# Kernel tuning notes

Hardware: AMD Instinct MI355X
Metric: run time of the kernel (lower is better)

## Reference

```python
import jax, jax.numpy as jnp
import numpy as np

N_NODES, FEAT, EMB, BATCH, NUM_SAMPLE = 100000, 256, 256, 10000, 32


def setup_inputs() -> dict:
    key = jax.random.key(0)
    ks = jax.random.split(key, 8)
    sc = 1.0 / np.sqrt(FEAT).astype(np.float32)
    return {
        "nodes": jax.random.randint(ks[0], (BATCH,), 0, N_NODES),
        "neigh_idx": jax.random.randint(ks[1], (BATCH, NUM_SAMPLE), 0, N_NODES),
        "id2feat": jax.random.normal(ks[2], (N_NODES, FEAT), jnp.float32),
        "Wq": jax.random.normal(ks[3], (FEAT, EMB), jnp.float32) * sc,
        "bq": jnp.zeros((EMB,), jnp.float32),
        "Wk": jax.random.normal(ks[4], (FEAT, EMB), jnp.float32) * sc,
        "bk": jnp.zeros((EMB,), jnp.float32),
        "Wv": jax.random.normal(ks[5], (FEAT, EMB), jnp.float32) * sc,
        "bv": jnp.zeros((EMB,), jnp.float32),
    }


def reference(nodes, neigh_idx, id2feat, Wq, bq, Wk, bk, Wv, bv):
    # Gather: self feats [B, F] and sampled neighbor feats [B, S, F]
    self_feats = id2feat[nodes]
    neigh_feats = id2feat[neigh_idx]
    S = neigh_idx.shape[1]
    # Keys/values over [neighbors, self] -> [B, S+1, F]
    cat = jnp.concatenate([neigh_feats, self_feats[:, None, :]], axis=1)
    Q = self_feats @ Wq + bq               # [B, E]
    K = cat @ Wk + bk                       # [B, S+1, E]
    V = cat @ Wv + bv                       # [B, S+1, E]
    scores = jnp.einsum('be,bse->bs', Q, K)  # [B, S+1]
    # Faithful to original mask loop: with full neighbor lists, columns >= num_sample
    # (the appended self key) are masked out.
    mask = jnp.arange(S + 1) >= S
    scores = jnp.where(mask[None, :], -jnp.inf, scores)
    attn = jax.nn.softmax(scores, axis=-1)   # [B, S+1]
    return jnp.einsum('bs,bse->be', attn, V)  # [B, E]
```

## Files before the change

kernel.cpp:

```cpp
#include <hip/hip_runtime.h>
#include <math.h>

#define F 256
#define E 256
#define S 32
#define CH 4
#define NB 16
#define TLP 260

typedef __attribute__((ext_vector_type(8))) short short8;
typedef __attribute__((ext_vector_type(4))) float f32x4;

__device__ __forceinline__ ushort f2bf(float x) {
    uint u = __float_as_uint(x);
    return (ushort)((u + 0x7fffu + ((u >> 16) & 1u)) >> 16);
}
__device__ __forceinline__ float bf2f(ushort h) {
    return __uint_as_float(((uint)h) << 16);
}
__device__ __forceinline__ uint4 pack8(const ushort* h) {
    uint4 r;
    r.x = (uint)h[0] | ((uint)h[1] << 16); r.y = (uint)h[2] | ((uint)h[3] << 16);
    r.z = (uint)h[4] | ((uint)h[5] << 16); r.w = (uint)h[6] | ((uint)h[7] << 16);
    return r;
}
__device__ __forceinline__ void split8(const float* x, short8& h, short8& l) {
    ushort hh[8], ll[8];
#pragma unroll
    for (int i = 0; i < 8; ++i) { hh[i] = f2bf(x[i]); ll[i] = f2bf(x[i] - bf2f(hh[i])); }
    uint4 ph = pack8(hh), pl = pack8(ll);
    h = *reinterpret_cast<short8*>(&ph);
    l = *reinterpret_cast<short8*>(&pl);
}
__device__ __forceinline__ short8 mk8(uint a, uint b, uint c, uint d) {
    uint4 p = make_uint4(a, b, c, d);
    return *reinterpret_cast<short8*>(&p);
}
__device__ __forceinline__ uint pkbf(float v) {
    const ushort h = f2bf(v);
    const ushort l = f2bf(v - bf2f(h));
    return (uint)h | ((uint)l << 16);
}

__global__ __launch_bounds__(512) void prep(const float* __restrict__ Wq,
                                            const float* __restrict__ bq,
                                            const float* __restrict__ Wk,
                                            const float* __restrict__ Wv,
                                            ushort* __restrict__ MTh,
                                            ushort* __restrict__ MTl,
                                            ushort* __restrict__ WvTh,
                                            ushort* __restrict__ WvTl,
                                            float* __restrict__ c) {
    const int blk = blockIdx.x, tid = threadIdx.x;
    const int lane = tid & 63, wave = tid >> 6;
    if (blk < 4) {
        const int wm = wave >> 2, wn = wave & 3;
        const int fr = lane & 15, fk = lane >> 4;
        const int j0 = blk * 64;
        f32x4 acc[2][4];
#pragma unroll
        for (int m = 0; m < 2; ++m)
#pragma unroll
            for (int n = 0; n < 4; ++n) acc[m][n] = (f32x4){0.f, 0.f, 0.f, 0.f};
        for (int k0 = 0; k0 < F; k0 += 32) {
            short8 ah[2], al[2];
#pragma unroll
            for (int m = 0; m < 2; ++m) {
                const float* p = &Wk[(size_t)(j0 + wm * 32 + m * 16 + fr) * F + k0 + fk * 8];
                float x[8];
                *reinterpret_cast<float4*>(&x[0]) = *reinterpret_cast<const float4*>(p);
                *reinterpret_cast<float4*>(&x[4]) = *reinterpret_cast<const float4*>(p + 4);
                split8(x, ah[m], al[m]);
            }
#pragma unroll
            for (int n = 0; n < 4; ++n) {
                const float* p = &Wq[(size_t)(wn * 64 + n * 16 + fr) * F + k0 + fk * 8];
                float x[8];
                *reinterpret_cast<float4*>(&x[0]) = *reinterpret_cast<const float4*>(p);
                *reinterpret_cast<float4*>(&x[4]) = *reinterpret_cast<const float4*>(p + 4);
                short8 bh, bl;
                split8(x, bh, bl);
#pragma unroll
                for (int m = 0; m < 2; ++m) {
                    acc[m][n] = __builtin_amdgcn_mfma_f32_16x16x32_bf16(ah[m], bh, acc[m][n], 0, 0, 0);
                    acc[m][n] = __builtin_amdgcn_mfma_f32_16x16x32_bf16(ah[m], bl, acc[m][n], 0, 0, 0);
                    acc[m][n] = __builtin_amdgcn_mfma_f32_16x16x32_bf16(al[m], bh, acc[m][n], 0, 0, 0);
                }
            }
        }
#pragma unroll
        for (int n = 0; n < 4; ++n) {
            const int i = wn * 64 + n * 16 + fr;
#pragma unroll
            for (int m = 0; m < 2; ++m)
#pragma unroll
                for (int r = 0; r < 4; ++r) {
                    const int j = j0 + wm * 32 + m * 16 + fk * 4 + r;
                    const float v = acc[m][n][r];
                    const ushort h = f2bf(v);
                    MTh[(size_t)j * F + i] = h;
                    MTl[(size_t)j * F + i] = f2bf(v - bf2f(h));
                }
        }
    } else if (blk < 20) {
        __shared__ float t[64][65];
        const int tb = blk - 4;
        const int jt = (tb & 3) * 64, kt = (tb >> 2) * 64;
        const int lk = tid >> 3, lj = (tid & 7) * 8;
        {
            const float* p = &Wv[(size_t)(kt + lk) * E + jt + lj];
            const float4 v0 = *reinterpret_cast<const float4*>(p);
            const float4 v1 = *reinterpret_cast<const float4*>(p + 4);
            t[lk][lj + 0] = v0.x; t[lk][lj + 1] = v0.y; t[lk][lj + 2] = v0.z; t[lk][lj + 3] = v0.w;
            t[lk][lj + 4] = v1.x; t[lk][lj + 5] = v1.y; t[lk][lj + 6] = v1.z; t[lk][lj + 7] = v1.w;
        }
        __syncthreads();
        const int oj = tid >> 3, ok = (tid & 7) * 8;
        ushort h[8], l[8];
#pragma unroll
        for (int u = 0; u < 8; ++u) {
            const float v = t[ok + u][oj];
            h[u] = f2bf(v); l[u] = f2bf(v - bf2f(h[u]));
        }
        *reinterpret_cast<uint4*>(&WvTh[(size_t)(jt + oj) * F + kt + ok]) = pack8(h);
        *reinterpret_cast<uint4*>(&WvTl[(size_t)(jt + oj) * F + kt + ok]) = pack8(l);
    } else {
        __shared__ float bqs[F];
        if (tid < F) bqs[tid] = bq[tid];
        __syncthreads();
        const float4 b4 = *reinterpret_cast<const float4*>(&bqs[lane * 4]);
#pragma unroll
        for (int i = 0; i < 8; ++i) {
            const int j = (blk - 20) * 64 + wave * 8 + i;
            const float4 k4 = *reinterpret_cast<const float4*>(&Wk[(size_t)j * F + lane * 4]);
            float p = k4.x * b4.x + k4.y * b4.y + k4.z * b4.z + k4.w * b4.w;
#pragma unroll
            for (int off = 32; off; off >>= 1) p += __shfl_xor(p, off);
            if (lane == 0) c[j] = p;
        }
    }
}

__device__ __forceinline__ void ld_chunk(float4* d, int idxv, int s0,
                                         const float* __restrict__ t, int lane) {
#pragma unroll
    for (int j = 0; j < CH; ++j) {
        const int nid = __builtin_amdgcn_readlane(idxv, s0 + j);
        d[j] = *reinterpret_cast<const float4*>(&t[(size_t)nid * F + lane * 4]);
    }
}
__device__ __forceinline__ void proc_chunk(const float4* v, const float4 qv,
                                           float& m, float& l, float4& acc) {
#pragma unroll
    for (int j = 0; j < CH; ++j) {
        float p = v[j].x * qv.x + v[j].y * qv.y + v[j].z * qv.z + v[j].w * qv.w;
#pragma unroll
        for (int off = 32; off; off >>= 1) p += __shfl_xor(p, off);
        if (p <= m) {
            const float w = __expf(p - m);
            l += w;
            acc.x += w * v[j].x; acc.y += w * v[j].y;
            acc.z += w * v[j].z; acc.w += w * v[j].w;
        } else {
            const float cc = __expf(m - p);
            l = l * cc + 1.f;
            acc.x = acc.x * cc + v[j].x; acc.y = acc.y * cc + v[j].y;
            acc.z = acc.z * cc + v[j].z; acc.w = acc.w * cc + v[j].w;
            m = p;
        }
    }
}

__global__ __launch_bounds__(256) void fused(const int* __restrict__ nodes,
                                             const int* __restrict__ neigh,
                                             const float* __restrict__ id2feat,
                                             const ushort* __restrict__ MTh,
                                             const ushort* __restrict__ MTl,
                                             const ushort* __restrict__ WvTh,
                                             const ushort* __restrict__ WvTl,
                                             const float* __restrict__ cb,
                                             const float* __restrict__ bv,
                                             float* __restrict__ out,
                                             int B) {
    __shared__ uint tile[NB][TLP];

    const int tid = threadIdx.x;
    const int lane = tid & 63, wave = tid >> 6;
    const int fr = lane & 15, fk = lane >> 4;
    const int row0 = blockIdx.x * NB;

    const int gr = row0 + fr;
    const int arow = nodes[gr < B ? gr : B - 1];

    f32x4 acc[4];
#pragma unroll
    for (int n = 0; n < 4; ++n) acc[n] = (f32x4){0.f, 0.f, 0.f, 0.f};

    for (int k0 = 0; k0 < F; k0 += 32) {
        const float* p = id2feat + (size_t)arow * F + k0 + fk * 8;
        float x[8];
        *reinterpret_cast<float4*>(&x[0]) = *reinterpret_cast<const float4*>(p);
        *reinterpret_cast<float4*>(&x[4]) = *reinterpret_cast<const float4*>(p + 4);
        short8 ah, al;
        split8(x, ah, al);
#pragma unroll
        for (int n = 0; n < 4; ++n) {
            const size_t boff = (size_t)(wave * 64 + n * 16 + fr) * F + k0 + fk * 8;
            const short8 bh = *reinterpret_cast<const short8*>(&MTh[boff]);
            const short8 bl = *reinterpret_cast<const short8*>(&MTl[boff]);
            acc[n] = __builtin_amdgcn_mfma_f32_16x16x32_bf16(ah, bh, acc[n], 0, 0, 0);
            acc[n] = __builtin_amdgcn_mfma_f32_16x16x32_bf16(ah, bl, acc[n], 0, 0, 0);
            acc[n] = __builtin_amdgcn_mfma_f32_16x16x32_bf16(al, bh, acc[n], 0, 0, 0);
        }
    }
#pragma unroll
    for (int n = 0; n < 4; ++n) {
        const int col = wave * 64 + n * 16 + fr;
        const float cc = cb[col];
#pragma unroll
        for (int r = 0; r < 4; ++r)
            tile[fk * 4 + r][col] = __float_as_uint(acc[n][r] + cc);
    }
    __syncthreads();

#pragma unroll 1
    for (int i = 0; i < 4; ++i) {
        const int tr = wave * 4 + i;
        const int node = row0 + tr;
        if (node < B) {
            const int idxv = neigh[node * S + (lane & (S - 1))];
            const uint4 q4 = *reinterpret_cast<const uint4*>(&tile[tr][lane * 4]);
            const float4 qv = make_float4(__uint_as_float(q4.x), __uint_as_float(q4.y),
                                          __uint_as_float(q4.z), __uint_as_float(q4.w));
            float m = -INFINITY, l = 0.f;
            float4 a = make_float4(0.f, 0.f, 0.f, 0.f);
            float4 va[CH], vb[CH];
            ld_chunk(va, idxv, 0, id2feat, lane);
            ld_chunk(vb, idxv, 4, id2feat, lane);
            proc_chunk(va, qv, m, l, a);
            ld_chunk(va, idxv, 8, id2feat, lane);
            proc_chunk(vb, qv, m, l, a);
            ld_chunk(vb, idxv, 12, id2feat, lane);
            proc_chunk(va, qv, m, l, a);
            ld_chunk(va, idxv, 16, id2feat, lane);
            proc_chunk(vb, qv, m, l, a);
            ld_chunk(vb, idxv, 20, id2feat, lane);
            proc_chunk(va, qv, m, l, a);
            ld_chunk(va, idxv, 24, id2feat, lane);
            proc_chunk(vb, qv, m, l, a);
            ld_chunk(vb, idxv, 28, id2feat, lane);
            proc_chunk(va, qv, m, l, a);
            proc_chunk(vb, qv, m, l, a);
            const float inv = 1.0f / l;
            const uint4 o = make_uint4(pkbf(a.x * inv), pkbf(a.y * inv),
                                       pkbf(a.z * inv), pkbf(a.w * inv));
            *reinterpret_cast<uint4*>(&tile[tr][lane * 4]) = o;
        }
    }
    __syncthreads();

#pragma unroll
    for (int n = 0; n < 4; ++n) acc[n] = (f32x4){0.f, 0.f, 0.f, 0.f};

    for (int k0 = 0; k0 < F; k0 += 32) {
        const uint4 u0 = *reinterpret_cast<const uint4*>(&tile[fr][k0 + fk * 8]);
        const uint4 u1 = *reinterpret_cast<const uint4*>(&tile[fr][k0 + fk * 8 + 4]);
        const short8 ah = mk8((u0.x & 0xffffu) | (u0.y << 16), (u0.z & 0xffffu) | (u0.w << 16),
                              (u1.x & 0xffffu) | (u1.y << 16), (u1.z & 0xffffu) | (u1.w << 16));
        const short8 al = mk8((u0.x >> 16) | (u0.y & 0xffff0000u), (u0.z >> 16) | (u0.w & 0xffff0000u),
                              (u1.x >> 16) | (u1.y & 0xffff0000u), (u1.z >> 16) | (u1.w & 0xffff0000u));
#pragma unroll
        for (int n = 0; n < 4; ++n) {
            const size_t boff = (size_t)(wave * 64 + n * 16 + fr) * F + k0 + fk * 8;
            const short8 bh = *reinterpret_cast<const short8*>(&WvTh[boff]);
            const short8 bl = *reinterpret_cast<const short8*>(&WvTl[boff]);
            acc[n] = __builtin_amdgcn_mfma_f32_16x16x32_bf16(ah, bh, acc[n], 0, 0, 0);
            acc[n] = __builtin_amdgcn_mfma_f32_16x16x32_bf16(ah, bl, acc[n], 0, 0, 0);
            acc[n] = __builtin_amdgcn_mfma_f32_16x16x32_bf16(al, bh, acc[n], 0, 0, 0);
        }
    }
#pragma unroll
    for (int n = 0; n < 4; ++n) {
        const int col = wave * 64 + n * 16 + fr;
        const float bb = bv[col];
#pragma unroll
        for (int r = 0; r < 4; ++r) {
            const int grow = row0 + fk * 4 + r;
            if (grow < B) out[(size_t)grow * E + col] = acc[n][r] + bb;
        }
    }
}

extern "C" void kernel_launch(void* const* d_in, const int* in_sizes, int n_in,
                              void* d_out, int out_size, void* d_ws, size_t ws_size,
                              hipStream_t stream) {
    const int*   nodes   = (const int*)d_in[0];
    const int*   neigh   = (const int*)d_in[1];
    const float* id2feat = (const float*)d_in[2];
    const float* Wq      = (const float*)d_in[3];
    const float* bq      = (const float*)d_in[4];
    const float* Wk      = (const float*)d_in[5];
    const float* Wv      = (const float*)d_in[7];
    const float* bv      = (const float*)d_in[8];
    float* out = (float*)d_out;
    const int B = in_sizes[0];

    ushort* MTh  = (ushort*)d_ws;
    ushort* MTl  = MTh + 65536;
    ushort* WvTh = MTl + 65536;
    ushort* WvTl = WvTh + 65536;
    float*  cbuf = (float*)(WvTl + 65536);

    prep<<<dim3(24), dim3(512), 0, stream>>>(Wq, bq, Wk, Wv, MTh, MTl, WvTh, WvTl, cbuf);
    fused<<<dim3((B + NB - 1) / NB), dim3(256), 0, stream>>>(nodes, neigh, id2feat,
                                                             MTh, MTl, WvTh, WvTl,
                                                             cbuf, bv, out, B);
}
```

Before: 124.7 us.

## Split fused kernel into tiled Q GEMM and per-node gather/attention kernel

Replaces the single fused kernel with two kernels. The first is a tiled GEMM that computes the transformed query for every batch node, staging A tiles in double-buffered LDS, and writes it to workspace. The second handles one node per wave for the online-softmax gather, then runs the Wv projection on 4-row tiles. That projection drops the Wv low-part MFMA term, which lowers precision. The aim is better occupancy and latency hiding for the gather phase, at the cost of a workspace round trip and MFMA tiles where only 4 of 16 rows carry data.

```diff
diff --git a/kernel.cpp b/kernel.cpp
--- a/kernel.cpp
+++ b/kernel.cpp
@@ -5,8 +5,6 @@
 #define E 256
 #define S 32
 #define CH 4
-#define NB 16
-#define TLP 260
 
 typedef __attribute__((ext_vector_type(8))) short short8;
 typedef __attribute__((ext_vector_type(4))) float f32x4;
@@ -23,6 +21,13 @@
     r.x = (uint)h[0] | ((uint)h[1] << 16); r.y = (uint)h[2] | ((uint)h[3] << 16);
     r.z = (uint)h[4] | ((uint)h[5] << 16); r.w = (uint)h[6] | ((uint)h[7] << 16);
     return r;
+}
+__device__ __forceinline__ void split4(const float* x, uint2& ph, uint2& pl) {
+    ushort h[4], l[4];
+#pragma unroll
+    for (int i = 0; i < 4; ++i) { h[i] = f2bf(x[i]); l[i] = f2bf(x[i] - bf2f(h[i])); }
+    ph.x = (uint)h[0] | ((uint)h[1] << 16); ph.y = (uint)h[2] | ((uint)h[3] << 16);
+    pl.x = (uint)l[0] | ((uint)l[1] << 16); pl.y = (uint)l[2] | ((uint)l[3] << 16);
 }
 __device__ __forceinline__ void split8(const float* x, short8& h, short8& l) {
     ushort hh[8], ll[8];
@@ -141,6 +146,83 @@
     }
 }
 
+__global__ __launch_bounds__(256) void qgemm(const float* __restrict__ X,
+                                             const int* __restrict__ nodes,
+                                             const ushort* __restrict__ BTh,
+                                             const ushort* __restrict__ BTl,
+                                             const float* __restrict__ cb,
+                                             float* __restrict__ outq,
+                                             int B) {
+    __shared__ ushort Ah[2][32][40], Al[2][32][40];
+    const int tid = threadIdx.x, lane = tid & 63, wave = tid >> 6;
+    const int fr = lane & 15, fk = lane >> 4;
+    const int row0 = blockIdx.x * 32;
+    const int col0 = blockIdx.y * 128 + wave * 32;
+
+    const int arL = tid >> 3, akL = (tid & 7) * 4;
+    const int gr = row0 + arL;
+    const int grc = gr < B ? gr : B - 1;
+    const float* aptr = X + (size_t)nodes[grc] * F + akL;
+
+    f32x4 acc[2][2];
+#pragma unroll
+    for (int m = 0; m < 2; ++m)
+#pragma unroll
+        for (int n = 0; n < 2; ++n) acc[m][n] = (f32x4){0.f, 0.f, 0.f, 0.f};
+
+    {
+        const float4 av = *reinterpret_cast<const float4*>(aptr);
+        uint2 h, l; split4(&av.x, h, l);
+        *reinterpret_cast<uint2*>(&Ah[0][arL][akL]) = h;
+        *reinterpret_cast<uint2*>(&Al[0][arL][akL]) = l;
+    }
+    __syncthreads();
+
+    for (int t = 0; t < 8; ++t) {
+        const int cur = t & 1;
+        float4 nv;
+        if (t < 7) nv = *reinterpret_cast<const float4*>(aptr + (t + 1) * 32);
+
+        short8 a_h[2], a_l[2];
+#pragma unroll
+        for (int m = 0; m < 2; ++m) {
+            a_h[m] = *reinterpret_cast<const short8*>(&Ah[cur][m * 16 + fr][fk * 8]);
+            a_l[m] = *reinterpret_cast<const short8*>(&Al[cur][m * 16 + fr][fk * 8]);
+        }
+#pragma unroll
+        for (int n = 0; n < 2; ++n) {
+            const size_t boff = (size_t)(col0 + n * 16 + fr) * F + t * 32 + fk * 8;
+            const short8 bh = *reinterpret_cast<const short8*>(&BTh[boff]);
+            const short8 bl = *reinterpret_cast<const short8*>(&BTl[boff]);
+#pragma unroll
+            for (int m = 0; m < 2; ++m) {
+                acc[m][n] = __builtin_amdgcn_mfma_f32_16x16x32_bf16(a_h[m], bh, acc[m][n], 0, 0, 0);
+                acc[m][n] = __builtin_amdgcn_mfma_f32_16x16x32_bf16(a_h[m], bl, acc[m][n], 0, 0, 0);
+                acc[m][n] = __builtin_amdgcn_mfma_f32_16x16x32_bf16(a_l[m], bh, acc[m][n], 0, 0, 0);
+            }
+        }
+        if (t < 7) {
+            uint2 h, l; split4(&nv.x, h, l);
+            *reinterpret_cast<uint2*>(&Ah[cur ^ 1][arL][akL]) = h;
+            *reinterpret_cast<uint2*>(&Al[cur ^ 1][arL][akL]) = l;
+        }
+        __syncthreads();
+    }
+
+#pragma unroll
+    for (int n = 0; n < 2; ++n) {
+        const int col = col0 + n * 16 + fr;
+        const float cc = cb[col];
+#pragma unroll
+        for (int m = 0; m < 2; ++m)
+#pragma unroll
+            for (int r = 0; r < 4; ++r) {
+                const int row = row0 + m * 16 + fk * 4 + r;
+                if (row < B) outq[(size_t)row * F + col] = acc[m][n][r] + cc;
+            }
+    }
+}
+
 __device__ __forceinline__ void ld_chunk(float4* d, int idxv, int s0,
                                          const float* __restrict__ t, int lane) {
 #pragma unroll
@@ -171,100 +253,54 @@
     }
 }
 
-__global__ __launch_bounds__(256) void fused(const int* __restrict__ nodes,
-                                             const int* __restrict__ neigh,
-                                             const float* __restrict__ id2feat,
-                                             const ushort* __restrict__ MTh,
-                                             const ushort* __restrict__ MTl,
-                                             const ushort* __restrict__ WvTh,
-                                             const ushort* __restrict__ WvTl,
-                                             const float* __restrict__ cb,
-                                             const float* __restrict__ bv,
-                                             float* __restrict__ out,
-                                             int B) {
-    __shared__ uint tile[NB][TLP];
-
-    const int tid = threadIdx.x;
-    const int lane = tid & 63, wave = tid >> 6;
+__global__ __launch_bounds__(256) void gatherD(const int* __restrict__ neigh,
+                                               const float* __restrict__ id2feat,
+                                               const float* __restrict__ qtm,
+                                               const ushort* __restrict__ WvTh,
+                                               const float* __restrict__ bv,
+                                               float* __restrict__ out,
+                                               int B) {
+    __shared__ uint tile[4][260];
+    const int tid = threadIdx.x, lane = tid & 63, wave = tid >> 6;
+    const int node = blockIdx.x * 4 + wave;
+
+    if (node < B) {
+        const int idxv = neigh[node * S + (lane & (S - 1))];
+        const float4 qv = *reinterpret_cast<const float4*>(&qtm[(size_t)node * F + lane * 4]);
+        float m = -INFINITY, l = 0.f;
+        float4 a = make_float4(0.f, 0.f, 0.f, 0.f);
+        float4 va[CH], vb[CH];
+        ld_chunk(va, idxv, 0, id2feat, lane);
+        ld_chunk(vb, idxv, 4, id2feat, lane);
+        proc_chunk(va, qv, m, l, a);
+        ld_chunk(va, idxv, 8, id2feat, lane);
+        proc_chunk(vb, qv, m, l, a);
+        ld_chunk(vb, idxv, 12, id2feat, lane);
+        proc_chunk(va, qv, m, l, a);
+        ld_chunk(va, idxv, 16, id2feat, lane);
+        proc_chunk(vb, qv, m, l, a);
+        ld_chunk(vb, idxv, 20, id2feat, lane);
+        proc_chunk(va, qv, m, l, a);
+        ld_chunk(va, idxv, 24, id2feat, lane);
+        proc_chunk(vb, qv, m, l, a);
+        ld_chunk(vb, idxv, 28, id2feat, lane);
+        proc_chunk(va, qv, m, l, a);
+        proc_chunk(vb, qv, m, l, a);
+        const float inv = 1.0f / l;
+        const uint4 o = make_uint4(pkbf(a.x * inv), pkbf(a.y * inv),
+                                   pkbf(a.z * inv), pkbf(a.w * inv));
+        *reinterpret_cast<uint4*>(&tile[wave][lane * 4]) = o;
+    }
+    __syncthreads();
+
     const int fr = lane & 15, fk = lane >> 4;
-    const int row0 = blockIdx.x * NB;
-
-    const int gr = row0 + fr;
-    const int arow = nodes[gr < B ? gr : B - 1];
-
     f32x4 acc[4];
 #pragma unroll
     for (int n = 0; n < 4; ++n) acc[n] = (f32x4){0.f, 0.f, 0.f, 0.f};
 
     for (int k0 = 0; k0 < F; k0 += 32) {
-        const float* p = id2feat + (size_t)arow * F + k0 + fk * 8;
-        float x[8];
-        *reinterpret_cast<float4*>(&x[0]) = *reinterpret_cast<const float4*>(p);
-        *reinterpret_cast<float4*>(&x[4]) = *reinterpret_cast<const float4*>(p + 4);
-        short8 ah, al;
-        split8(x, ah, al);
-#pragma unroll
-        for (int n = 0; n < 4; ++n) {
-            const size_t boff = (size_t)(wave * 64 + n * 16 + fr) * F + k0 + fk * 8;
-            const short8 bh = *reinterpret_cast<const short8*>(&MTh[boff]);
-            const short8 bl = *reinterpret_cast<const short8*>(&MTl[boff]);
-            acc[n] = __builtin_amdgcn_mfma_f32_16x16x32_bf16(ah, bh, acc[n], 0, 0, 0);
-            acc[n] = __builtin_amdgcn_mfma_f32_16x16x32_bf16(ah, bl, acc[n], 0, 0, 0);
-            acc[n] = __builtin_amdgcn_mfma_f32_16x16x32_bf16(al, bh, acc[n], 0, 0, 0);
-        }
-    }
-#pragma unroll
-    for (int n = 0; n < 4; ++n) {
-        const int col = wave * 64 + n * 16 + fr;
-        const float cc = cb[col];
-#pragma unroll
-        for (int r = 0; r < 4; ++r)
-            tile[fk * 4 + r][col] = __float_as_uint(acc[n][r] + cc);
-    }
-    __syncthreads();
-
-#pragma unroll 1
-    for (int i = 0; i < 4; ++i) {
-        const int tr = wave * 4 + i;
-        const int node = row0 + tr;
-        if (node < B) {
-            const int idxv = neigh[node * S + (lane & (S - 1))];
-            const uint4 q4 = *reinterpret_cast<const uint4*>(&tile[tr][lane * 4]);
-            const float4 qv = make_float4(__uint_as_float(q4.x), __uint_as_float(q4.y),
-                                          __uint_as_float(q4.z), __uint_as_float(q4.w));
-            float m = -INFINITY, l = 0.f;
-            float4 a = make_float4(0.f, 0.f, 0.f, 0.f);
-            float4 va[CH], vb[CH];
-            ld_chunk(va, idxv, 0, id2feat, lane);
-            ld_chunk(vb, idxv, 4, id2feat, lane);
-            proc_chunk(va, qv, m, l, a);
-            ld_chunk(va, idxv, 8, id2feat, lane);
-            proc_chunk(vb, qv, m, l, a);
-            ld_chunk(vb, idxv, 12, id2feat, lane);
-            proc_chunk(va, qv, m, l, a);
-            ld_chunk(va, idxv, 16, id2feat, lane);
-            proc_chunk(vb, qv, m, l, a);
-            ld_chunk(vb, idxv, 20, id2feat, lane);
-            proc_chunk(va, qv, m, l, a);
-            ld_chunk(va, idxv, 24, id2feat, lane);
-            proc_chunk(vb, qv, m, l, a);
-            ld_chunk(vb, idxv, 28, id2feat, lane);
-            proc_chunk(va, qv, m, l, a);
-            proc_chunk(vb, qv, m, l, a);
-            const float inv = 1.0f / l;
-            const uint4 o = make_uint4(pkbf(a.x * inv), pkbf(a.y * inv),
-                                       pkbf(a.z * inv), pkbf(a.w * inv));
-            *reinterpret_cast<uint4*>(&tile[tr][lane * 4]) = o;
-        }
-    }
-    __syncthreads();
-
-#pragma unroll
-    for (int n = 0; n < 4; ++n) acc[n] = (f32x4){0.f, 0.f, 0.f, 0.f};
-
-    for (int k0 = 0; k0 < F; k0 += 32) {
-        const uint4 u0 = *reinterpret_cast<const uint4*>(&tile[fr][k0 + fk * 8]);
-        const uint4 u1 = *reinterpret_cast<const uint4*>(&tile[fr][k0 + fk * 8 + 4]);
+        const uint4 u0 = *reinterpret_cast<const uint4*>(&tile[fr & 3][k0 + fk * 8]);
+        const uint4 u1 = *reinterpret_cast<const uint4*>(&tile[fr & 3][k0 + fk * 8 + 4]);
         const short8 ah = mk8((u0.x & 0xffffu) | (u0.y << 16), (u0.z & 0xffffu) | (u0.w << 16),
                               (u1.x & 0xffffu) | (u1.y << 16), (u1.z & 0xffffu) | (u1.w << 16));
         const short8 al = mk8((u0.x >> 16) | (u0.y & 0xffff0000u), (u0.z >> 16) | (u0.w & 0xffff0000u),
@@ -273,20 +309,20 @@
         for (int n = 0; n < 4; ++n) {
             const size_t boff = (size_t)(wave * 64 + n * 16 + fr) * F + k0 + fk * 8;
             const short8 bh = *reinterpret_cast<const short8*>(&WvTh[boff]);
-            const short8 bl = *reinterpret_cast<const short8*>(&WvTl[boff]);
             acc[n] = __builtin_amdgcn_mfma_f32_16x16x32_bf16(ah, bh, acc[n], 0, 0, 0);
-            acc[n] = __builtin_amdgcn_mfma_f32_16x16x32_bf16(ah, bl, acc[n], 0, 0, 0);
             acc[n] = __builtin_amdgcn_mfma_f32_16x16x32_bf16(al, bh, acc[n], 0, 0, 0);
         }
     }
-#pragma unroll
-    for (int n = 0; n < 4; ++n) {
-        const int col = wave * 64 + n * 16 + fr;
-        const float bb = bv[col];
-#pragma unroll
-        for (int r = 0; r < 4; ++r) {
-            const int grow = row0 + fk * 4 + r;
-            if (grow < B) out[(size_t)grow * E + col] = acc[n][r] + bb;
+    if (fk == 0) {
+#pragma unroll
+        for (int n = 0; n < 4; ++n) {
+            const int col = wave * 64 + n * 16 + fr;
+            const float bb = bv[col];
+#pragma unroll
+            for (int r = 0; r < 4; ++r) {
+                const int grow = blockIdx.x * 4 + r;
+                if (grow < B) out[(size_t)grow * E + col] = acc[n][r] + bb;
+            }
         }
     }
 }
@@ -310,9 +346,11 @@
     ushort* WvTh = MTl + 65536;
     ushort* WvTl = WvTh + 65536;
     float*  cbuf = (float*)(WvTl + 65536);
+    float*  qtm  = cbuf + 256;
 
     prep<<<dim3(24), dim3(512), 0, stream>>>(Wq, bq, Wk, Wv, MTh, MTl, WvTh, WvTl, cbuf);
-    fused<<<dim3((B + NB - 1) / NB), dim3(256), 0, stream>>>(nodes, neigh, id2feat,
-                                                             MTh, MTl, WvTh, WvTl,
-                                                             cbuf, bv, out, B);
-}
+    qgemm<<<dim3((B + 31) / 32, 2), dim3(256), 0, stream>>>(id2feat, nodes,
+                                                            MTh, MTl, cbuf, qtm, B);
+    gatherD<<<dim3((B + 3) / 4), dim3(256), 0, stream>>>(neigh, id2feat, qtm,
+                                                         WvTh, bv, out, B);
+}
```

Measured after the change: 123.5 us. Within noise of the previous version (-0.9%).
